# Performance work log

Hardware: AMD Instinct MI355X
Metric: run time of the kernel (lower is better)

Reference implementation:

```python
import jax, jax.numpy as jnp
import numpy as np

B, R, D = 16, 360, 64  # batch, roi_num, input_dim


def setup_inputs() -> dict:
    key = jax.random.key(0)
    ks = jax.random.split(key, 5)
    scale_out = 1.0 / np.sqrt(2 * D)
    scale_cat = 1.0 / np.sqrt(D)
    return {
        "x": jax.random.normal(ks[0], (B, R, D), dtype=jnp.float32),
        # torch Linear stores [out,in]; we store transposed [in,out] for x @ W
        "W_out": jax.random.uniform(ks[1], (2 * D, D), jnp.float32, -scale_out, scale_out),
        "b_out": jax.random.uniform(ks[2], (D,), jnp.float32, -scale_out, scale_out),
        "W_cat": jax.random.uniform(ks[3], (D, 1), jnp.float32, -scale_cat, scale_cat),
        "b_cat": jax.random.uniform(ks[4], (1,), jnp.float32, -scale_cat, scale_cat),
    }


def reference(x, W_out, b_out, W_cat, b_cat):
    b, r, _ = x.shape
    # rel_rec/rel_send are one-hot over np.where(ones([R,R])) -> row-major
    # rows = repeat(arange(R), R) (receivers), cols = tile(arange(R), R) (senders).
    rec_idx = jnp.repeat(jnp.arange(r), r)   # [R*R]
    send_idx = jnp.tile(jnp.arange(r), r)    # [R*R]
    receivers = x[:, rec_idx]                # [B, R*R, D] gather, not dense GEMM
    senders = x[:, send_idx]                 # [B, R*R, D]
    h = jnp.concatenate([senders, receivers], axis=2)        # [B, R*R, 2D]
    h = jax.nn.relu(jnp.einsum('bef,fd->bed', h, W_out) + b_out)  # [B, R*R, D]
    out = jax.nn.relu(jnp.einsum('bed,do->beo', h, W_cat) + b_cat)  # [B, R*R, 1]
    return out.reshape(b, r, r, -1)
```

## Files before the change

### kernel.cpp

```cpp
#include <hip/hip_runtime.h>

#define BATCH 16
#define RR    360
#define DD    64
#define RPB   16
#define TI    8

typedef _Float16 h2 __attribute__((ext_vector_type(2)));

__global__ __launch_bounds__(256) void precompute_st(
    const float* __restrict__ x, const float* __restrict__ Wout,
    const float* __restrict__ bout, const float* __restrict__ wcat,
    _Float16* __restrict__ s_h, _Float16* __restrict__ t_h,
    _Float16* __restrict__ w_h)
{
    __shared__ float WTs[DD * 68];
    __shared__ float WTt[DD * 68];
    __shared__ float xl[RPB * DD];

    const int tid  = threadIdx.x;
    const int row0 = blockIdx.x * RPB;

    #pragma unroll
    for (int it = 0; it < 32; ++it) {
        const int e = tid + it * 256;
        const int f = e >> 6, d = e & 63;
        const float v = Wout[e];
        if (f < DD) WTs[d * 68 + f] = v;
        else        WTt[d * 68 + (f - DD)] = v;
    }
    {
        const float4* x4 = (const float4*)(x + (size_t)row0 * DD);
        ((float4*)xl)[tid] = x4[tid];
    }
    if (blockIdx.x == 0 && tid < DD) w_h[tid] = (_Float16)wcat[tid];

    __syncthreads();

    const int d   = tid & 63;
    const int sub = tid >> 6;
    const float bv = bout[d];

    float ws[DD], wt[DD];
    #pragma unroll
    for (int k = 0; k < DD / 4; ++k) {
        const float4 a = *(const float4*)&WTs[d * 68 + 4 * k];
        ws[4*k] = a.x; ws[4*k+1] = a.y; ws[4*k+2] = a.z; ws[4*k+3] = a.w;
        const float4 c = *(const float4*)&WTt[d * 68 + 4 * k];
        wt[4*k] = c.x; wt[4*k+1] = c.y; wt[4*k+2] = c.z; wt[4*k+3] = c.w;
    }

    #pragma unroll
    for (int q = 0; q < 4; ++q) {
        const int r = sub * 4 + q;
        float sa = 0.f, ta = bv;
        #pragma unroll
        for (int k = 0; k < DD / 4; ++k) {
            const float4 xv = *(const float4*)&xl[r * DD + 4 * k];
            sa = fmaf(xv.x, ws[4*k  ], sa);  ta = fmaf(xv.x, wt[4*k  ], ta);
            sa = fmaf(xv.y, ws[4*k+1], sa);  ta = fmaf(xv.y, wt[4*k+1], ta);
            sa = fmaf(xv.z, ws[4*k+2], sa);  ta = fmaf(xv.z, wt[4*k+2], ta);
            sa = fmaf(xv.w, ws[4*k+3], sa);  ta = fmaf(xv.w, wt[4*k+3], ta);
        }
        s_h[(size_t)(row0 + r) * DD + d] = (_Float16)sa;
        t_h[(size_t)(row0 + r) * DD + d] = (_Float16)ta;
    }
}

__global__ __launch_bounds__(384) void pairwise_out(
    const h2* __restrict__ s_h, const h2* __restrict__ t_h,
    const h2* __restrict__ w_h, const float* __restrict__ bcat,
    float* __restrict__ out)
{
    const int tid = threadIdx.x;
    const int b   = blockIdx.y;
    const int i0  = blockIdx.x * TI;
    const float bc = bcat[0];

    h2 wl[DD / 2];
    #pragma unroll
    for (int k = 0; k < DD / 2; ++k) wl[k] = w_h[k];

    const int j = tid;
    if (j >= RR) return;

    h2 sr[DD / 2];
    const h2* srow = s_h + ((size_t)b * RR + j) * (DD / 2);
    #pragma unroll
    for (int k = 0; k < DD / 2; ++k) sr[k] = srow[k];

    h2 zero; zero.x = (_Float16)0; zero.y = (_Float16)0;

    float* orow = out + ((size_t)b * RR * RR + (size_t)i0 * RR + j);
    const h2* tbase = t_h + ((size_t)b * RR + i0) * (DD / 2);

    #pragma unroll
    for (int ii = 0; ii < TI; ++ii) {
        const h2* trow = tbase + ii * (DD / 2);
        float acc = bc;
        #pragma unroll
        for (int k = 0; k < DD / 2; ++k) {
            h2 p = sr[k] + trow[k];
            p = __builtin_elementwise_max(p, zero);
#if __has_builtin(__builtin_amdgcn_fdot2)
            acc = __builtin_amdgcn_fdot2(p, wl[k], acc, false);
#else
            acc = fmaf((float)p.x, (float)wl[k].x, acc);
            acc = fmaf((float)p.y, (float)wl[k].y, acc);
#endif
        }
        acc = acc > 0.f ? acc : 0.f;
        orow[(size_t)ii * RR] = acc;
    }
}

extern "C" void kernel_launch(void* const* d_in, const int* in_sizes, int n_in,
                              void* d_out, int out_size, void* d_ws, size_t ws_size,
                              hipStream_t stream) {
    const float* x    = (const float*)d_in[0];
    const float* Wout = (const float*)d_in[1];
    const float* bout = (const float*)d_in[2];
    const float* Wcat = (const float*)d_in[3];
    const float* bcat = (const float*)d_in[4];
    float* out = (float*)d_out;

    _Float16* s_h = (_Float16*)d_ws;
    _Float16* t_h = s_h + (size_t)BATCH * RR * DD;
    _Float16* w_h = t_h + (size_t)BATCH * RR * DD;

    precompute_st<<<dim3(BATCH * RR / RPB), dim3(256), 0, stream>>>(
        x, Wout, bout, Wcat, s_h, t_h, w_h);
    pairwise_out<<<dim3(RR / TI, BATCH), dim3(384), 0, stream>>>(
        (const h2*)s_h, (const h2*)t_h, (const h2*)w_h, bcat, out);
}
```

Baseline: 78.88 us.

## Drop LDS staging in precompute, use global device buffers, split dot accumulators

```diff
diff --git a/kernel.cpp b/kernel.cpp
--- a/kernel.cpp
+++ b/kernel.cpp
@@ -8,74 +8,58 @@
 
 typedef _Float16 h2 __attribute__((ext_vector_type(2)));
 
+__device__ _Float16 g_s[BATCH * RR * DD];
+__device__ _Float16 g_t[BATCH * RR * DD];
+__device__ _Float16 g_w[DD];
+
 __global__ __launch_bounds__(256) void precompute_st(
     const float* __restrict__ x, const float* __restrict__ Wout,
-    const float* __restrict__ bout, const float* __restrict__ wcat,
-    _Float16* __restrict__ s_h, _Float16* __restrict__ t_h,
-    _Float16* __restrict__ w_h)
+    const float* __restrict__ bout, const float* __restrict__ wcat)
 {
-    __shared__ float WTs[DD * 68];
-    __shared__ float WTt[DD * 68];
-    __shared__ float xl[RPB * DD];
-
     const int tid  = threadIdx.x;
+    const int d    = tid & 63;
+    const int subu = __builtin_amdgcn_readfirstlane(tid >> 6);
     const int row0 = blockIdx.x * RPB;
 
-    #pragma unroll
-    for (int it = 0; it < 32; ++it) {
-        const int e = tid + it * 256;
-        const int f = e >> 6, d = e & 63;
-        const float v = Wout[e];
-        if (f < DD) WTs[d * 68 + f] = v;
-        else        WTt[d * 68 + (f - DD)] = v;
-    }
-    {
-        const float4* x4 = (const float4*)(x + (size_t)row0 * DD);
-        ((float4*)xl)[tid] = x4[tid];
-    }
-    if (blockIdx.x == 0 && tid < DD) w_h[tid] = (_Float16)wcat[tid];
-
-    __syncthreads();
-
-    const int d   = tid & 63;
-    const int sub = tid >> 6;
-    const float bv = bout[d];
+    if (blockIdx.x == 0 && tid < DD) g_w[tid] = (_Float16)wcat[tid];
 
     float ws[DD], wt[DD];
     #pragma unroll
-    for (int k = 0; k < DD / 4; ++k) {
-        const float4 a = *(const float4*)&WTs[d * 68 + 4 * k];
-        ws[4*k] = a.x; ws[4*k+1] = a.y; ws[4*k+2] = a.z; ws[4*k+3] = a.w;
-        const float4 c = *(const float4*)&WTt[d * 68 + 4 * k];
-        wt[4*k] = c.x; wt[4*k+1] = c.y; wt[4*k+2] = c.z; wt[4*k+3] = c.w;
+    for (int f = 0; f < DD; ++f) {
+        ws[f] = Wout[f * DD + d];
+        wt[f] = Wout[(DD + f) * DD + d];
     }
+    const float bv = bout[d];
 
     #pragma unroll
-    for (int q = 0; q < 4; ++q) {
-        const int r = sub * 4 + q;
-        float sa = 0.f, ta = bv;
+    for (int q = 0; q < RPB / 4; ++q) {
+        const int r = row0 + subu * (RPB / 4) + q;
+        const float* xr = x + (size_t)r * DD;
+        float s0 = 0.f, s1 = 0.f, t0 = bv, t1 = 0.f;
         #pragma unroll
-        for (int k = 0; k < DD / 4; ++k) {
-            const float4 xv = *(const float4*)&xl[r * DD + 4 * k];
-            sa = fmaf(xv.x, ws[4*k  ], sa);  ta = fmaf(xv.x, wt[4*k  ], ta);
-            sa = fmaf(xv.y, ws[4*k+1], sa);  ta = fmaf(xv.y, wt[4*k+1], ta);
-            sa = fmaf(xv.z, ws[4*k+2], sa);  ta = fmaf(xv.z, wt[4*k+2], ta);
-            sa = fmaf(xv.w, ws[4*k+3], sa);  ta = fmaf(xv.w, wt[4*k+3], ta);
+        for (int k = 0; k < DD; k += 2) {
+            const float x0 = xr[k], x1 = xr[k + 1];
+            s0 = fmaf(x0, ws[k],     s0);
+            s1 = fmaf(x1, ws[k + 1], s1);
+            t0 = fmaf(x0, wt[k],     t0);
+            t1 = fmaf(x1, wt[k + 1], t1);
         }
-        s_h[(size_t)(row0 + r) * DD + d] = (_Float16)sa;
-        t_h[(size_t)(row0 + r) * DD + d] = (_Float16)ta;
+        g_s[(size_t)r * DD + d] = (_Float16)(s0 + s1);
+        g_t[(size_t)r * DD + d] = (_Float16)(t0 + t1);
     }
 }
 
 __global__ __launch_bounds__(384) void pairwise_out(
-    const h2* __restrict__ s_h, const h2* __restrict__ t_h,
-    const h2* __restrict__ w_h, const float* __restrict__ bcat,
-    float* __restrict__ out)
+    const float* __restrict__ bcat, float* __restrict__ out)
 {
     const int tid = threadIdx.x;
     const int b   = blockIdx.y;
     const int i0  = blockIdx.x * TI;
     const float bc = bcat[0];
+
+    const h2* s_h = (const h2*)g_s;
+    const h2* t_h = (const h2*)g_t;
+    const h2* w_h = (const h2*)g_w;
 
     h2 wl[DD / 2];
     #pragma unroll
@@ -97,26 +81,32 @@
     #pragma unroll
     for (int ii = 0; ii < TI; ++ii) {
         const h2* trow = tbase + ii * (DD / 2);
-        float acc = bc;
+        float a0 = bc, a1 = 0.f;
         #pragma unroll
-        for (int k = 0; k < DD / 2; ++k) {
-            h2 p = sr[k] + trow[k];
-            p = __builtin_elementwise_max(p, zero);
+        for (int k = 0; k < DD / 2; k += 2) {
+            h2 p0 = sr[k]   + trow[k];
+            h2 p1 = sr[k+1] + trow[k+1];
+            p0 = __builtin_elementwise_max(p0, zero);
+            p1 = __builtin_elementwise_max(p1, zero);
 #if __has_builtin(__builtin_amdgcn_fdot2)
-            acc = __builtin_amdgcn_fdot2(p, wl[k], acc, false);
+            a0 = __builtin_amdgcn_fdot2(p0, wl[k],   a0, false);
+            a1 = __builtin_amdgcn_fdot2(p1, wl[k+1], a1, false);
 #else
-            acc = fmaf((float)p.x, (float)wl[k].x, acc);
-            acc = fmaf((float)p.y, (float)wl[k].y, acc);
+            a0 = fmaf((float)p0.x, (float)wl[k].x,   a0);
+            a0 = fmaf((float)p0.y, (float)wl[k].y,   a0);
+            a1 = fmaf((float)p1.x, (float)wl[k+1].x, a1);
+            a1 = fmaf((float)p1.y, (float)wl[k+1].y, a1);
 #endif
         }
-        acc = acc > 0.f ? acc : 0.f;
-        orow[(size_t)ii * RR] = acc;
+        const float acc = a0 + a1;
+        orow[(size_t)ii * RR] = acc > 0.f ? acc : 0.f;
     }
 }
 
 extern "C" void kernel_launch(void* const* d_in, const int* in_sizes, int n_in,
                               void* d_out, int out_size, void* d_ws, size_t ws_size,
                               hipStream_t stream) {
+    (void)d_ws; (void)ws_size;
     const float* x    = (const float*)d_in[0];
     const float* Wout = (const float*)d_in[1];
     const float* bout = (const float*)d_in[2];
@@ -124,12 +114,8 @@
     const float* bcat = (const float*)d_in[4];
     float* out = (float*)d_out;
 
-    _Float16* s_h = (_Float16*)d_ws;
-    _Float16* t_h = s_h + (size_t)BATCH * RR * DD;
-    _Float16* w_h = t_h + (size_t)BATCH * RR * DD;
-
     precompute_st<<<dim3(BATCH * RR / RPB), dim3(256), 0, stream>>>(
-        x, Wout, bout, Wcat, s_h, t_h, w_h);
+        x, Wout, bout, Wcat);
     pairwise_out<<<dim3(RR / TI, BATCH), dim3(384), 0, stream>>>(
-        (const h2*)s_h, (const h2*)t_h, (const h2*)w_h, bcat, out);
+        bcat, out);
 }
```

Result: slower. 81.86 us (+3.8%).
